# Performance work log

Measured on AMD Instinct MI355X. Metric: run time of the kernel, lower is better.

## Reference

```python
import jax, jax.numpy as jnp
import numpy as np

M, D_H, D_K, D_V = 8, 512, 64, 64
B, N = 16, 1024

def _xavier(key, shape, gain=1.414):
    fan_in, fan_out = shape[-2], shape[-1]
    limit = gain * (6.0 / (fan_in + fan_out)) ** 0.5
    return jax.random.uniform(key, shape, jnp.float32, -limit, limit)

def setup_inputs() -> dict:
    key = jax.random.key(0)
    kH, kq, kk, kv, ko = jax.random.split(key, 5)
    return {
        "H": jax.random.normal(kH, (B, N, D_H), jnp.float32),
        "W_Q": _xavier(kq, (M, D_H, D_K)),
        "W_K": _xavier(kk, (M, D_H, D_K)),
        "W_V": _xavier(kv, (M, D_H, D_V)),
        "W_O": _xavier(ko, (M, D_V, D_H)),
    }

def reference(H, W_Q, W_K, W_V, W_O):
    # H: [B, n, d_h]; per-head projections -> [B, M, n, d_k/d_v]
    Q = jnp.einsum('bnd,mdq->bmnq', H, W_Q)
    K = jnp.einsum('bnd,mdk->bmnk', H, W_K)
    V = jnp.einsum('bnd,mdv->bmnv', H, W_V)
    scale = 1.0 / jnp.sqrt(jnp.float32(W_K.shape[-1]))
    U = scale * jnp.einsum('bmnq,bmkq->bmnk', Q, K)  # [B, M, n, n]
    A = jax.nn.softmax(U, axis=-1)
    Hp = jnp.einsum('bmnk,bmkv->bmnv', A, V)          # [B, M, n, d_v]
    # per-head output projection then sum over heads (dim=-3)
    return jnp.einsum('bmnv,mvd->bnd', Hp, W_O)       # [B, n, d_h]
```

## Files before the change

### kernel.cpp

```cpp
#include <hip/hip_runtime.h>
#include <hip/hip_bf16.h>

typedef __attribute__((ext_vector_type(8))) short bf16x8;
typedef __attribute__((ext_vector_type(4))) float f32x4;
typedef __attribute__((ext_vector_type(16))) float f32x16;
typedef __attribute__((ext_vector_type(2))) unsigned uint2v;

__device__ __forceinline__ ushort f2bf(float f) {
  union { float f; unsigned u; } v; v.f = f;
  unsigned r = v.u + 0x7FFFu + ((v.u >> 16) & 1u);
  return (ushort)(r >> 16);
}

__device__ __forceinline__ float exp2_(float x) {
#if __has_builtin(__builtin_amdgcn_exp2f)
  return __builtin_amdgcn_exp2f(x);
#else
  return exp2f(x);
#endif
}

__device__ __forceinline__ unsigned cvtpk(float lo, float hi) {
  unsigned r;
  asm("v_cvt_pk_bf16_f32 %0, %1, %2" : "=v"(r) : "v"(lo), "v"(hi));
  return r;
}

__device__ __forceinline__ uint2v lane32_swap(unsigned a, unsigned b) {
#if __has_builtin(__builtin_amdgcn_permlane32_swap)
  return __builtin_amdgcn_permlane32_swap(a, b, false, false);
#else
  unsigned sa = (unsigned)__shfl_xor((int)a, 32);
  unsigned sb = (unsigned)__shfl_xor((int)b, 32);
  bool lo = ((threadIdx.x & 32) == 0);
  uint2v r;
  r.x = lo ? a : sb;
  r.y = lo ? sa : b;
  return r;
#endif
}

#define QSCALE 0.18033688011112042f

__global__ void __launch_bounds__(256) cast_h_kernel(const float* __restrict__ src,
                                                     ushort* __restrict__ dst) {
  int i = (blockIdx.x * 256 + threadIdx.x) * 8;
  float4 a = *(const float4*)(src + i);
  float4 b = *(const float4*)(src + i + 4);
  uint4 o;
  o.x = f2bf(a.x) | ((unsigned)f2bf(a.y) << 16);
  o.y = f2bf(a.z) | ((unsigned)f2bf(a.w) << 16);
  o.z = f2bf(b.x) | ((unsigned)f2bf(b.y) << 16);
  o.w = f2bf(b.z) | ((unsigned)f2bf(b.w) << 16);
  *(uint4*)(dst + i) = o;
}

__global__ void __launch_bounds__(256) pack_wqkv_kernel(const float* __restrict__ WQ,
                                                        const float* __restrict__ WK,
                                                        const float* __restrict__ WV,
                                                        ushort* __restrict__ dst) {
  int t = blockIdx.x * 256 + threadIdx.x;
  int j = t >> 9, d = t & 511;
  int m = j / 192, r = j % 192, which = r >> 6, dk = r & 63;
  const float* W = (which == 0) ? WQ : (which == 1) ? WK : WV;
  dst[t] = f2bf(W[(m * 512 + d) * 64 + dk]);
}

__global__ void __launch_bounds__(256) pack_wo_kernel(const float* __restrict__ WO,
                                                      ushort* __restrict__ dst) {
  int t = blockIdx.x * 256 + threadIdx.x;
  int j = t >> 9, mv = t & 511;
  dst[t] = f2bf(WO[mv * 512 + j]);
}

template <int EPI>
__global__ void __launch_bounds__(256) gemm_bt_kernel(
    const ushort* __restrict__ A, const ushort* __restrict__ Bt,
    float* __restrict__ C, int Kdim, int Ncols,
    ushort* __restrict__ Qo, ushort* __restrict__ Ko, ushort* __restrict__ Vo) {
  __shared__ __align__(16) ushort As[128][72];
  __shared__ __align__(16) ushort Bs[128][72];
  const int tid = threadIdx.x;
  const int lane = tid & 63, w = tid >> 6;
  const int wr = w >> 1, wc = w & 1;
  const int brow = blockIdx.y * 128, bcol = blockIdx.x * 128;

  f32x4 acc[4][4];
  const f32x4 z4 = {0.f, 0.f, 0.f, 0.f};
#pragma unroll
  for (int i = 0; i < 4; ++i)
#pragma unroll
    for (int j = 0; j < 4; ++j) acc[i][j] = z4;

  for (int k0 = 0; k0 < Kdim; k0 += 64) {
    __syncthreads();
#pragma unroll
    for (int i = 0; i < 4; ++i) {
      int c = tid + i * 256;
      int row = c >> 3, cc = (c & 7) * 8;
      *(uint4*)&As[row][cc] = *(const uint4*)(A + (size_t)(brow + row) * Kdim + k0 + cc);
      *(uint4*)&Bs[row][cc] = *(const uint4*)(Bt + (size_t)(bcol + row) * Kdim + k0 + cc);
    }
    __syncthreads();
#pragma unroll
    for (int kk = 0; kk < 64; kk += 32) {
      bf16x8 a[4], b[4];
#pragma unroll
      for (int i = 0; i < 4; ++i)
        a[i] = *(const bf16x8*)&As[wr * 64 + i * 16 + (lane & 15)][kk + (lane >> 4) * 8];
#pragma unroll
      for (int j = 0; j < 4; ++j)
        b[j] = *(const bf16x8*)&Bs[wc * 64 + j * 16 + (lane & 15)][kk + (lane >> 4) * 8];
#pragma unroll
      for (int i = 0; i < 4; ++i)
#pragma unroll
        for (int j = 0; j < 4; ++j)
          acc[i][j] = __builtin_amdgcn_mfma_f32_16x16x32_bf16(a[i], b[j], acc[i][j], 0, 0, 0);
    }
  }

#pragma unroll
  for (int i = 0; i < 4; ++i) {
    int row0 = brow + wr * 64 + i * 16 + (lane >> 4) * 4;
#pragma unroll
    for (int j = 0; j < 4; ++j) {
      int col = bcol + wc * 64 + j * 16 + (lane & 15);
      if (EPI == 0) {
#pragma unroll
        for (int q = 0; q < 4; ++q)
          C[(size_t)(row0 + q) * Ncols + col] = acc[i][j][q];
      } else {
        int m = col / 192, r = col % 192, which = r >> 6, dk = r & 63;
        ushort* base = (which == 0) ? Qo : (which == 1) ? Ko : Vo;
        float cs = (which == 0) ? QSCALE : 1.0f;
#pragma unroll
        for (int q = 0; q < 4; ++q) {
          int row = row0 + q;
          int b = row >> 10, n = row & 1023;
          base[(size_t)((b * 8 + m) * 1024 + n) * 64 + dk] = f2bf(acc[i][j][q] * cs);
        }
      }
    }
  }
}

__global__ void __launch_bounds__(256) transpose_v_kernel(const ushort* __restrict__ V,
                                                          ushort* __restrict__ Vt) {
  __shared__ __align__(16) ushort T[64][72];
  int bm = blockIdx.x >> 4, nt = blockIdx.x & 15;
  const ushort* src = V + (size_t)bm * 65536 + nt * 64 * 64;
  int tid = threadIdx.x;
#pragma unroll
  for (int i = 0; i < 2; ++i) {
    int c = tid + i * 256;
    int row = c >> 3, cc = (c & 7) * 8;
    *(uint4*)&T[row][cc] = *(const uint4*)(src + c * 8);
  }
  __syncthreads();
  int v = tid >> 2, nn0 = (tid & 3) * 16;
  ushort tmp[16];
#pragma unroll
  for (int k = 0; k < 16; ++k) tmp[k] = T[nn0 + k][v];
  ushort* dst = Vt + (size_t)bm * 65536 + v * 1024 + nt * 64 + nn0;
  *(uint4*)(dst + 0) = *(uint4*)&tmp[0];
  *(uint4*)(dst + 8) = *(uint4*)&tmp[8];
}

__global__ void __launch_bounds__(256, 2) attn_kernel(const ushort* __restrict__ Q,
                                                      const ushort* __restrict__ K,
                                                      const ushort* __restrict__ Vt,
                                                      ushort* __restrict__ Hp) {
  __shared__ __align__(16) ushort Ks[2][64 * 64];
  __shared__ __align__(16) ushort Vs[2][64 * 64];

  int wk = (blockIdx.x & 7) * 64 + (blockIdx.x >> 3);
  const int bm = wk >> 2, qt = wk & 3;
  const int b = bm >> 3, m = bm & 7;
  const int tid = threadIdx.x, lane = tid & 63, w = tid >> 6;
  const int hi = lane >> 5, l31 = lane & 31;
  const ushort* Qp = Q + (size_t)bm * 65536;
  const ushort* Kp = K + (size_t)bm * 65536;
  const ushort* Vp = Vt + (size_t)bm * 65536;
  const int qw = qt * 256 + w * 64;

  bf16x8 qb[2][4];
#pragma unroll
  for (int qs = 0; qs < 2; ++qs)
#pragma unroll
    for (int s = 0; s < 4; ++s)
      qb[qs][s] = *(const bf16x8*)(Qp + (size_t)(qw + qs * 32 + l31) * 64 + s * 16 + hi * 8);

  f32x16 oacc[2][2];
#pragma unroll
  for (int qs = 0; qs < 2; ++qs)
#pragma unroll
    for (int vj = 0; vj < 2; ++vj)
#pragma unroll
      for (int r = 0; r < 16; ++r) oacc[qs][vj][r] = 0.f;
  float mrun[2] = {-1e30f, -1e30f}, lrun[2] = {0.f, 0.f};

  const int sr = tid >> 2, sc4 = (tid & 3) << 4;
  const unsigned bo0 = ((unsigned)(sc4 * 2)) ^ (((unsigned)(sr & 7)) << 4);

  {
    uint4 k0 = *(const uint4*)(Kp + (size_t)sr * 64 + sc4);
    uint4 k1 = *(const uint4*)(Kp + (size_t)sr * 64 + sc4 + 8);
    uint4 v0 = *(const uint4*)(Vp + (size_t)sr * 1024 + sc4);
    uint4 v1 = *(const uint4*)(Vp + (size_t)sr * 1024 + sc4 + 8);
    char* kd = (char*)&Ks[0][sr * 64];
    char* vd = (char*)&Vs[0][sr * 64];
    *(uint4*)(kd + bo0) = k0; *(uint4*)(kd + (bo0 ^ 16)) = k1;
    *(uint4*)(vd + bo0) = v0; *(uint4*)(vd + (bo0 ^ 16)) = v1;
  }
  __syncthreads();

  int cur = 0;
  for (int kt = 0; kt < 16; ++kt) {
    uint4 k0, k1, v0, v1;
    const bool pf = (kt < 15);
    if (pf) {
      int n0 = (kt + 1) * 64;
      k0 = *(const uint4*)(Kp + (size_t)(n0 + sr) * 64 + sc4);
      k1 = *(const uint4*)(Kp + (size_t)(n0 + sr) * 64 + sc4 + 8);
      v0 = *(const uint4*)(Vp + (size_t)sr * 1024 + n0 + sc4);
      v1 = *(const uint4*)(Vp + (size_t)sr * 1024 + n0 + sc4 + 8);
    }

    const ushort* kbase = &Ks[cur][0];
    bf16x8 kA[2][4];
#pragma unroll
    for (int ja = 0; ja < 2; ++ja) {
      int row = ja * 32 + l31;
      const char* kr = (const char*)(kbase + row * 64);
#pragma unroll
      for (int s = 0; s < 4; ++s)
        kA[ja][s] = *(const bf16x8*)(kr + (((unsigned)(s * 32 + hi * 16)) ^ (((unsigned)(row & 7)) << 4)));
    }

    f32x16 st[2][2];
#pragma unroll
    for (int qs = 0; qs < 2; ++qs)
#pragma unroll
      for (int ja = 0; ja < 2; ++ja) {
#pragma unroll
        for (int r = 0; r < 16; ++r) st[qs][ja][r] = 0.f;
#pragma unroll
        for (int s = 0; s < 4; ++s)
          st[qs][ja] = __builtin_amdgcn_mfma_f32_32x32x16_bf16(kA[ja][s], qb[qs][s], st[qs][ja], 0, 0, 0);
      }

    bf16x8 pb[2][4];
#pragma unroll
    for (int qs = 0; qs < 2; ++qs) {
      float tm[16];
#pragma unroll
      for (int r = 0; r < 16; ++r) tm[r] = fmaxf(st[qs][0][r], st[qs][1][r]);
#pragma unroll
      for (int sd = 8; sd >= 1; sd >>= 1)
#pragma unroll
        for (int r = 0; r < sd; ++r) tm[r] = fmaxf(tm[r], tm[r + sd]);
      float mx = fmaxf(tm[0], __shfl_xor(tm[0], 32));
      float mnew = fmaxf(mrun[qs], mx);
      float scal = exp2_(mrun[qs] - mnew);
      mrun[qs] = mnew;
#pragma unroll
      for (int ja = 0; ja < 2; ++ja)
#pragma unroll
        for (int r = 0; r < 16; ++r)
          st[qs][ja][r] = exp2_(st[qs][ja][r] - mnew);
      float ts[16];
#pragma unroll
      for (int r = 0; r < 16; ++r) ts[r] = st[qs][0][r] + st[qs][1][r];
#pragma unroll
      for (int sd = 8; sd >= 1; sd >>= 1)
#pragma unroll
        for (int r = 0; r < sd; ++r) ts[r] += ts[r + sd];
      float rs = ts[0] + __shfl_xor(ts[0], 32);
      lrun[qs] = lrun[qs] * scal + rs;
#pragma unroll
      for (int vj = 0; vj < 2; ++vj)
#pragma unroll
        for (int r = 0; r < 16; ++r) oacc[qs][vj][r] *= scal;

#pragma unroll
      for (int ja = 0; ja < 2; ++ja)
#pragma unroll
        for (int g = 0; g < 2; ++g) {
          unsigned x0 = cvtpk(st[qs][ja][g * 8 + 0], st[qs][ja][g * 8 + 1]);
          unsigned x1 = cvtpk(st[qs][ja][g * 8 + 2], st[qs][ja][g * 8 + 3]);
          unsigned y0 = cvtpk(st[qs][ja][g * 8 + 4], st[qs][ja][g * 8 + 5]);
          unsigned y1 = cvtpk(st[qs][ja][g * 8 + 6], st[qs][ja][g * 8 + 7]);
          uint2v s0 = lane32_swap(x0, y0);
          uint2v s1 = lane32_swap(x1, y1);
          uint4 wv; wv.x = s0.x; wv.y = s1.x; wv.z = s0.y; wv.w = s1.y;
          pb[qs][ja * 2 + g] = *(bf16x8*)&wv;
        }
    }

    const ushort* vbase = &Vs[cur][0];
#pragma unroll
    for (int vj = 0; vj < 2; ++vj) {
      int row = vj * 32 + l31;
      const char* vr = (const char*)(vbase + row * 64);
      bf16x8 va[4];
#pragma unroll
      for (int ks = 0; ks < 4; ++ks)
        va[ks] = *(const bf16x8*)(vr + (((unsigned)(ks * 32 + hi * 16)) ^ (((unsigned)(row & 7)) << 4)));
#pragma unroll
      for (int qs = 0; qs < 2; ++qs)
#pragma unroll
        for (int ks = 0; ks < 4; ++ks)
          oacc[qs][vj] = __builtin_amdgcn_mfma_f32_32x32x16_bf16(va[ks], pb[qs][ks], oacc[qs][vj], 0, 0, 0);
    }

    if (pf) {
      char* kd = (char*)&Ks[cur ^ 1][sr * 64];
      char* vd = (char*)&Vs[cur ^ 1][sr * 64];
      *(uint4*)(kd + bo0) = k0; *(uint4*)(kd + (bo0 ^ 16)) = k1;
      *(uint4*)(vd + bo0) = v0; *(uint4*)(vd + (bo0 ^ 16)) = v1;
    }
    __syncthreads();
    cur ^= 1;
  }

#pragma unroll
  for (int qs = 0; qs < 2; ++qs) {
    float linv = 1.0f / lrun[qs];
    int q = qw + qs * 32 + l31;
    size_t ro = ((size_t)b * 1024 + q) * 512 + m * 64;
#pragma unroll
    for (int vj = 0; vj < 2; ++vj)
#pragma unroll
      for (int t4 = 0; t4 < 4; ++t4) {
        ushort4 o;
        o.x = f2bf(oacc[qs][vj][t4 * 4 + 0] * linv);
        o.y = f2bf(oacc[qs][vj][t4 * 4 + 1] * linv);
        o.z = f2bf(oacc[qs][vj][t4 * 4 + 2] * linv);
        o.w = f2bf(oacc[qs][vj][t4 * 4 + 3] * linv);
        *(ushort4*)(Hp + ro + vj * 32 + t4 * 8 + hi * 4) = o;
      }
  }
}

extern "C" void kernel_launch(void* const* d_in, const int* in_sizes, int n_in,
                              void* d_out, int out_size, void* d_ws, size_t ws_size,
                              hipStream_t stream) {
  const float* H  = (const float*)d_in[0];
  const float* WQ = (const float*)d_in[1];
  const float* WK = (const float*)d_in[2];
  const float* WV = (const float*)d_in[3];
  const float* WO = (const float*)d_in[4];
  float* out = (float*)d_out;

  ushort* ws   = (ushort*)d_ws;
  ushort* Hb   = ws;
  ushort* Wqkv = Hb + 16384 * 512;
  ushort* Wo   = Wqkv + 1536 * 512;
  ushort* Qb   = Wo + 512 * 512;
  ushort* Kb   = Qb + 128 * 1024 * 64;
  ushort* Vb   = Kb + 128 * 1024 * 64;
  ushort* Vtb  = Vb + 128 * 1024 * 64;
  ushort* Hp   = Vtb + 128 * 1024 * 64;

  cast_h_kernel<<<4096, 256, 0, stream>>>(H, Hb);
  pack_wqkv_kernel<<<3072, 256, 0, stream>>>(WQ, WK, WV, Wqkv);
  pack_wo_kernel<<<1024, 256, 0, stream>>>(WO, Wo);
  gemm_bt_kernel<1><<<dim3(12, 128), 256, 0, stream>>>(Hb, Wqkv, nullptr, 512, 1536,
                                                       Qb, Kb, Vb);
  transpose_v_kernel<<<2048, 256, 0, stream>>>(Vb, Vtb);
  attn_kernel<<<512, 256, 0, stream>>>(Qb, Kb, Vtb, Hp);
  gemm_bt_kernel<0><<<dim3(4, 128), 256, 0, stream>>>(Hp, Wo, out, 512, 512,
                                                      nullptr, nullptr, nullptr);
}
```

Baseline: 137.6 us.

## Fuse V transpose into QKV GEMM, use LDS direct loads, lazy-rescale softmax

The QKV GEMM now writes V already transposed, which removes the separate transpose kernel and its round trip through memory. Its tile loads now go straight from global memory into LDS via global_load_lds, with an unpadded layout. The attention kernel halves the queries per wave and doubles the grid, raising occupancy to 3 blocks. It folds the running-max subtraction into the MFMA accumulator input and rescales only when the max exceeds a threshold of 10. The row sums are computed with an MFMA against a ones vector instead of shuffle reductions. The lazy rescaling relies on scores staying bounded, and the unpadded LDS layout in the GEMM may cause bank conflicts.

```diff
diff --git a/kernel.cpp b/kernel.cpp
--- a/kernel.cpp
+++ b/kernel.cpp
@@ -40,6 +40,12 @@
 #endif
 }
 
+__device__ __forceinline__ void gload_lds16(const ushort* g, ushort* l) {
+  __builtin_amdgcn_global_load_lds(
+      (const __attribute__((address_space(1))) void*)g,
+      (__attribute__((address_space(3))) void*)l, 16, 0, 0);
+}
+
 #define QSCALE 0.18033688011112042f
 
 __global__ void __launch_bounds__(256) cast_h_kernel(const float* __restrict__ src,
@@ -77,14 +83,19 @@
 __global__ void __launch_bounds__(256) gemm_bt_kernel(
     const ushort* __restrict__ A, const ushort* __restrict__ Bt,
     float* __restrict__ C, int Kdim, int Ncols,
-    ushort* __restrict__ Qo, ushort* __restrict__ Ko, ushort* __restrict__ Vo) {
-  __shared__ __align__(16) ushort As[128][72];
-  __shared__ __align__(16) ushort Bs[128][72];
+    ushort* __restrict__ Qo, ushort* __restrict__ Ko, ushort* __restrict__ Vto) {
+  __shared__ __align__(16) ushort As[128 * 64];
+  __shared__ __align__(16) ushort Bs[128 * 64];
   const int tid = threadIdx.x;
   const int lane = tid & 63, w = tid >> 6;
   const int wr = w >> 1, wc = w & 1;
   const int brow = blockIdx.y * 128, bcol = blockIdx.x * 128;
 
+  const int srow = w * 32 + (lane >> 3);
+  const int scol = (lane & 7) * 8;
+  const ushort* ga = A + (size_t)(brow + srow) * Kdim + scol;
+  const ushort* gb = Bt + (size_t)(bcol + srow) * Kdim + scol;
+
   f32x4 acc[4][4];
   const f32x4 z4 = {0.f, 0.f, 0.f, 0.f};
 #pragma unroll
@@ -95,11 +106,9 @@
   for (int k0 = 0; k0 < Kdim; k0 += 64) {
     __syncthreads();
 #pragma unroll
-    for (int i = 0; i < 4; ++i) {
-      int c = tid + i * 256;
-      int row = c >> 3, cc = (c & 7) * 8;
-      *(uint4*)&As[row][cc] = *(const uint4*)(A + (size_t)(brow + row) * Kdim + k0 + cc);
-      *(uint4*)&Bs[row][cc] = *(const uint4*)(Bt + (size_t)(bcol + row) * Kdim + k0 + cc);
+    for (int t = 0; t < 4; ++t) {
+      gload_lds16(ga + k0 + t * 8 * Kdim, &As[(w * 32 + t * 8) * 64]);
+      gload_lds16(gb + k0 + t * 8 * Kdim, &Bs[(w * 32 + t * 8) * 64]);
     }
     __syncthreads();
 #pragma unroll
@@ -107,10 +116,10 @@
       bf16x8 a[4], b[4];
 #pragma unroll
       for (int i = 0; i < 4; ++i)
-        a[i] = *(const bf16x8*)&As[wr * 64 + i * 16 + (lane & 15)][kk + (lane >> 4) * 8];
+        a[i] = *(const bf16x8*)&As[(wr * 64 + i * 16 + (lane & 15)) * 64 + kk + (lane >> 4) * 8];
 #pragma unroll
       for (int j = 0; j < 4; ++j)
-        b[j] = *(const bf16x8*)&Bs[wc * 64 + j * 16 + (lane & 15)][kk + (lane >> 4) * 8];
+        b[j] = *(const bf16x8*)&Bs[(wc * 64 + j * 16 + (lane & 15)) * 64 + kk + (lane >> 4) * 8];
 #pragma unroll
       for (int i = 0; i < 4; ++i)
 #pragma unroll
@@ -131,73 +140,56 @@
           C[(size_t)(row0 + q) * Ncols + col] = acc[i][j][q];
       } else {
         int m = col / 192, r = col % 192, which = r >> 6, dk = r & 63;
-        ushort* base = (which == 0) ? Qo : (which == 1) ? Ko : Vo;
-        float cs = (which == 0) ? QSCALE : 1.0f;
-#pragma unroll
-        for (int q = 0; q < 4; ++q) {
-          int row = row0 + q;
-          int b = row >> 10, n = row & 1023;
-          base[(size_t)((b * 8 + m) * 1024 + n) * 64 + dk] = f2bf(acc[i][j][q] * cs);
+        int bb = row0 >> 10, n = row0 & 1023;
+        if (which == 2) {
+          ushort4 o;
+          o.x = f2bf(acc[i][j][0]);
+          o.y = f2bf(acc[i][j][1]);
+          o.z = f2bf(acc[i][j][2]);
+          o.w = f2bf(acc[i][j][3]);
+          *(ushort4*)(Vto + ((size_t)(bb * 8 + m) << 16) + (size_t)dk * 1024 + n) = o;
+        } else {
+          ushort* base = (which == 0) ? Qo : Ko;
+          float cs = (which == 0) ? QSCALE : 1.0f;
+#pragma unroll
+          for (int q = 0; q < 4; ++q)
+            base[(size_t)((bb * 8 + m) * 1024 + (n + q)) * 64 + dk] = f2bf(acc[i][j][q] * cs);
         }
       }
     }
   }
 }
 
-__global__ void __launch_bounds__(256) transpose_v_kernel(const ushort* __restrict__ V,
-                                                          ushort* __restrict__ Vt) {
-  __shared__ __align__(16) ushort T[64][72];
-  int bm = blockIdx.x >> 4, nt = blockIdx.x & 15;
-  const ushort* src = V + (size_t)bm * 65536 + nt * 64 * 64;
-  int tid = threadIdx.x;
-#pragma unroll
-  for (int i = 0; i < 2; ++i) {
-    int c = tid + i * 256;
-    int row = c >> 3, cc = (c & 7) * 8;
-    *(uint4*)&T[row][cc] = *(const uint4*)(src + c * 8);
-  }
-  __syncthreads();
-  int v = tid >> 2, nn0 = (tid & 3) * 16;
-  ushort tmp[16];
-#pragma unroll
-  for (int k = 0; k < 16; ++k) tmp[k] = T[nn0 + k][v];
-  ushort* dst = Vt + (size_t)bm * 65536 + v * 1024 + nt * 64 + nn0;
-  *(uint4*)(dst + 0) = *(uint4*)&tmp[0];
-  *(uint4*)(dst + 8) = *(uint4*)&tmp[8];
-}
-
-__global__ void __launch_bounds__(256, 2) attn_kernel(const ushort* __restrict__ Q,
+__global__ void __launch_bounds__(256, 3) attn_kernel(const ushort* __restrict__ Q,
                                                       const ushort* __restrict__ K,
                                                       const ushort* __restrict__ Vt,
                                                       ushort* __restrict__ Hp) {
   __shared__ __align__(16) ushort Ks[2][64 * 64];
   __shared__ __align__(16) ushort Vs[2][64 * 64];
 
-  int wk = (blockIdx.x & 7) * 64 + (blockIdx.x >> 3);
-  const int bm = wk >> 2, qt = wk & 3;
+  int wk = (blockIdx.x & 7) * 128 + (blockIdx.x >> 3);
+  const int bm = wk >> 3, qt = wk & 7;
   const int b = bm >> 3, m = bm & 7;
   const int tid = threadIdx.x, lane = tid & 63, w = tid >> 6;
   const int hi = lane >> 5, l31 = lane & 31;
   const ushort* Qp = Q + (size_t)bm * 65536;
   const ushort* Kp = K + (size_t)bm * 65536;
   const ushort* Vp = Vt + (size_t)bm * 65536;
-  const int qw = qt * 256 + w * 64;
-
-  bf16x8 qb[2][4];
-#pragma unroll
-  for (int qs = 0; qs < 2; ++qs)
-#pragma unroll
-    for (int s = 0; s < 4; ++s)
-      qb[qs][s] = *(const bf16x8*)(Qp + (size_t)(qw + qs * 32 + l31) * 64 + s * 16 + hi * 8);
-
-  f32x16 oacc[2][2];
-#pragma unroll
-  for (int qs = 0; qs < 2; ++qs)
-#pragma unroll
-    for (int vj = 0; vj < 2; ++vj)
-#pragma unroll
-      for (int r = 0; r < 16; ++r) oacc[qs][vj][r] = 0.f;
-  float mrun[2] = {-1e30f, -1e30f}, lrun[2] = {0.f, 0.f};
+  const int qw = qt * 128 + w * 32;
+
+  bf16x8 qb[4];
+#pragma unroll
+  for (int s = 0; s < 4; ++s)
+    qb[s] = *(const bf16x8*)(Qp + (size_t)(qw + l31) * 64 + s * 16 + hi * 8);
+
+  bf16x8 ones;
+#pragma unroll
+  for (int j = 0; j < 8; ++j) ones[j] = (short)0x3F80;
+
+  f32x16 oacc[2], lacc;
+#pragma unroll
+  for (int r = 0; r < 16; ++r) { oacc[0][r] = 0.f; oacc[1][r] = 0.f; lacc[r] = 0.f; }
+  float mrun = 0.f;
 
   const int sr = tid >> 2, sc4 = (tid & 3) << 4;
   const unsigned bo0 = ((unsigned)(sc4 * 2)) ^ (((unsigned)(sr & 7)) << 4);
@@ -237,65 +229,60 @@
         kA[ja][s] = *(const bf16x8*)(kr + (((unsigned)(s * 32 + hi * 16)) ^ (((unsigned)(row & 7)) << 4)));
     }
 
-    f32x16 st[2][2];
-#pragma unroll
-    for (int qs = 0; qs < 2; ++qs)
-#pragma unroll
-      for (int ja = 0; ja < 2; ++ja) {
-#pragma unroll
-        for (int r = 0; r < 16; ++r) st[qs][ja][r] = 0.f;
-#pragma unroll
-        for (int s = 0; s < 4; ++s)
-          st[qs][ja] = __builtin_amdgcn_mfma_f32_32x32x16_bf16(kA[ja][s], qb[qs][s], st[qs][ja], 0, 0, 0);
+    f32x16 cin;
+#pragma unroll
+    for (int r = 0; r < 16; ++r) cin[r] = -mrun;
+    f32x16 st0 = __builtin_amdgcn_mfma_f32_32x32x16_bf16(kA[0][0], qb[0], cin, 0, 0, 0);
+    f32x16 st1 = __builtin_amdgcn_mfma_f32_32x32x16_bf16(kA[1][0], qb[0], cin, 0, 0, 0);
+#pragma unroll
+    for (int s = 1; s < 4; ++s) {
+      st0 = __builtin_amdgcn_mfma_f32_32x32x16_bf16(kA[0][s], qb[s], st0, 0, 0, 0);
+      st1 = __builtin_amdgcn_mfma_f32_32x32x16_bf16(kA[1][s], qb[s], st1, 0, 0, 0);
+    }
+
+    float t[8];
+#pragma unroll
+    for (int r = 0; r < 8; ++r)
+      t[r] = fmaxf(fmaxf(st0[r], st0[r + 8]), fmaxf(st1[r], st1[r + 8]));
+    t[0] = fmaxf(fmaxf(t[0], t[4]), fmaxf(t[1], t[5]));
+    t[2] = fmaxf(fmaxf(t[2], t[6]), fmaxf(t[3], t[7]));
+    float mx = fmaxf(t[0], t[2]);
+    mx = fmaxf(mx, __shfl_xor(mx, 32));
+
+    if (__any(mx > 10.f)) {
+      float d = (mx > 10.f) ? mx : 0.f;
+      float scal = exp2_(-d);
+      mrun += d;
+#pragma unroll
+      for (int r = 0; r < 16; ++r) { st0[r] -= d; st1[r] -= d; }
+#pragma unroll
+      for (int r = 0; r < 16; ++r) { oacc[0][r] *= scal; oacc[1][r] *= scal; }
+      lacc[0] *= scal;
+    }
+
+#pragma unroll
+    for (int r = 0; r < 16; ++r) { st0[r] = exp2_(st0[r]); st1[r] = exp2_(st1[r]); }
+
+    bf16x8 pb[4];
+#pragma unroll
+    for (int ja = 0; ja < 2; ++ja) {
+      const f32x16& sj = ja ? st1 : st0;
+#pragma unroll
+      for (int g = 0; g < 2; ++g) {
+        unsigned x0 = cvtpk(sj[g * 8 + 0], sj[g * 8 + 1]);
+        unsigned x1 = cvtpk(sj[g * 8 + 2], sj[g * 8 + 3]);
+        unsigned y0 = cvtpk(sj[g * 8 + 4], sj[g * 8 + 5]);
+        unsigned y1 = cvtpk(sj[g * 8 + 6], sj[g * 8 + 7]);
+        uint2v s0 = lane32_swap(x0, y0);
+        uint2v s1 = lane32_swap(x1, y1);
+        uint4 wv; wv.x = s0.x; wv.y = s1.x; wv.z = s0.y; wv.w = s1.y;
+        pb[ja * 2 + g] = *(bf16x8*)&wv;
       }
-
-    bf16x8 pb[2][4];
-#pragma unroll
-    for (int qs = 0; qs < 2; ++qs) {
-      float tm[16];
-#pragma unroll
-      for (int r = 0; r < 16; ++r) tm[r] = fmaxf(st[qs][0][r], st[qs][1][r]);
-#pragma unroll
-      for (int sd = 8; sd >= 1; sd >>= 1)
-#pragma unroll
-        for (int r = 0; r < sd; ++r) tm[r] = fmaxf(tm[r], tm[r + sd]);
-      float mx = fmaxf(tm[0], __shfl_xor(tm[0], 32));
-      float mnew = fmaxf(mrun[qs], mx);
-      float scal = exp2_(mrun[qs] - mnew);
-      mrun[qs] = mnew;
-#pragma unroll
-      for (int ja = 0; ja < 2; ++ja)
-#pragma unroll
-        for (int r = 0; r < 16; ++r)
-          st[qs][ja][r] = exp2_(st[qs][ja][r] - mnew);
-      float ts[16];
-#pragma unroll
-      for (int r = 0; r < 16; ++r) ts[r] = st[qs][0][r] + st[qs][1][r];
-#pragma unroll
-      for (int sd = 8; sd >= 1; sd >>= 1)
-#pragma unroll
-        for (int r = 0; r < sd; ++r) ts[r] += ts[r + sd];
-      float rs = ts[0] + __shfl_xor(ts[0], 32);
-      lrun[qs] = lrun[qs] * scal + rs;
-#pragma unroll
-      for (int vj = 0; vj < 2; ++vj)
-#pragma unroll
-        for (int r = 0; r < 16; ++r) oacc[qs][vj][r] *= scal;
-
-#pragma unroll
-      for (int ja = 0; ja < 2; ++ja)
-#pragma unroll
-        for (int g = 0; g < 2; ++g) {
-          unsigned x0 = cvtpk(st[qs][ja][g * 8 + 0], st[qs][ja][g * 8 + 1]);
-          unsigned x1 = cvtpk(st[qs][ja][g * 8 + 2], st[qs][ja][g * 8 + 3]);
-          unsigned y0 = cvtpk(st[qs][ja][g * 8 + 4], st[qs][ja][g * 8 + 5]);
-          unsigned y1 = cvtpk(st[qs][ja][g * 8 + 6], st[qs][ja][g * 8 + 7]);
-          uint2v s0 = lane32_swap(x0, y0);
-          uint2v s1 = lane32_swap(x1, y1);
-          uint4 wv; wv.x = s0.x; wv.y = s1.x; wv.z = s0.y; wv.w = s1.y;
-          pb[qs][ja * 2 + g] = *(bf16x8*)&wv;
-        }
-    }
+    }
+
+#pragma unroll
+    for (int ks = 0; ks < 4; ++ks)
+      lacc = __builtin_amdgcn_mfma_f32_32x32x16_bf16(ones, pb[ks], lacc, 0, 0, 0);
 
     const ushort* vbase = &Vs[cur][0];
 #pragma unroll
@@ -307,10 +294,8 @@
       for (int ks = 0; ks < 4; ++ks)
         va[ks] = *(const bf16x8*)(vr + (((unsigned)(ks * 32 + hi * 16)) ^ (((unsigned)(row & 7)) << 4)));
 #pragma unroll
-      for (int qs = 0; qs < 2; ++qs)
-#pragma unroll
-        for (int ks = 0; ks < 4; ++ks)
-          oacc[qs][vj] = __builtin_amdgcn_mfma_f32_32x32x16_bf16(va[ks], pb[qs][ks], oacc[qs][vj], 0, 0, 0);
+      for (int ks = 0; ks < 4; ++ks)
+        oacc[vj] = __builtin_amdgcn_mfma_f32_32x32x16_bf16(va[ks], pb[ks], oacc[vj], 0, 0, 0);
     }
 
     if (pf) {
@@ -323,23 +308,20 @@
     cur ^= 1;
   }
 
-#pragma unroll
-  for (int qs = 0; qs < 2; ++qs) {
-    float linv = 1.0f / lrun[qs];
-    int q = qw + qs * 32 + l31;
-    size_t ro = ((size_t)b * 1024 + q) * 512 + m * 64;
-#pragma unroll
-    for (int vj = 0; vj < 2; ++vj)
-#pragma unroll
-      for (int t4 = 0; t4 < 4; ++t4) {
-        ushort4 o;
-        o.x = f2bf(oacc[qs][vj][t4 * 4 + 0] * linv);
-        o.y = f2bf(oacc[qs][vj][t4 * 4 + 1] * linv);
-        o.z = f2bf(oacc[qs][vj][t4 * 4 + 2] * linv);
-        o.w = f2bf(oacc[qs][vj][t4 * 4 + 3] * linv);
-        *(ushort4*)(Hp + ro + vj * 32 + t4 * 8 + hi * 4) = o;
-      }
-  }
+  float linv = 1.0f / lacc[0];
+  int q = qw + l31;
+  size_t ro = ((size_t)b * 1024 + q) * 512 + m * 64;
+#pragma unroll
+  for (int vj = 0; vj < 2; ++vj)
+#pragma unroll
+    for (int t4 = 0; t4 < 4; ++t4) {
+      ushort4 o;
+      o.x = f2bf(oacc[vj][t4 * 4 + 0] * linv);
+      o.y = f2bf(oacc[vj][t4 * 4 + 1] * linv);
+      o.z = f2bf(oacc[vj][t4 * 4 + 2] * linv);
+      o.w = f2bf(oacc[vj][t4 * 4 + 3] * linv);
+      *(ushort4*)(Hp + ro + vj * 32 + t4 * 8 + hi * 4) = o;
+    }
 }
 
 extern "C" void kernel_launch(void* const* d_in, const int* in_sizes, int n_in,
@@ -358,17 +340,15 @@
   ushort* Wo   = Wqkv + 1536 * 512;
   ushort* Qb   = Wo + 512 * 512;
   ushort* Kb   = Qb + 128 * 1024 * 64;
-  ushort* Vb   = Kb + 128 * 1024 * 64;
-  ushort* Vtb  = Vb + 128 * 1024 * 64;
+  ushort* Vtb  = Kb + 128 * 1024 * 64;
   ushort* Hp   = Vtb + 128 * 1024 * 64;
 
   cast_h_kernel<<<4096, 256, 0, stream>>>(H, Hb);
   pack_wqkv_kernel<<<3072, 256, 0, stream>>>(WQ, WK, WV, Wqkv);
   pack_wo_kernel<<<1024, 256, 0, stream>>>(WO, Wo);
   gemm_bt_kernel<1><<<dim3(12, 128), 256, 0, stream>>>(Hb, Wqkv, nullptr, 512, 1536,
-                                                       Qb, Kb, Vb);
-  transpose_v_kernel<<<2048, 256, 0, stream>>>(Vb, Vtb);
-  attn_kernel<<<512, 256, 0, stream>>>(Qb, Kb, Vtb, Hp);
+                                                       Qb, Kb, Vtb);
+  attn_kernel<<<1024, 256, 0, stream>>>(Qb, Kb, Vtb, Hp);
   gemm_bt_kernel<0><<<dim3(4, 128), 256, 0, stream>>>(Hp, Wo, out, 512, 512,
                                                       nullptr, nullptr, nullptr);
 }
```

Measured after the change: 141.7 us. +3.0%, slower.

## Fuse prep kernels, use direct global-to-LDS loads in GEMM, lazy softmax rescale

Applied to the files above, without the earlier changes.

Merges the three cast/pack kernels into one launch to cut launch overhead. The GEMM tile loads now go straight from global memory into LDS via global_load_lds and drop the padded LDS layout. The attention kernel folds the running max into the MFMA accumulator init and rescales only when the max grows past a threshold, which removes the per-tile exp and rescale of the accumulators. The unpadded LDS layout may add bank conflicts, and the lazy max relies on scores staying within a bounded range.

```diff
diff --git a/kernel.cpp b/kernel.cpp
--- a/kernel.cpp
+++ b/kernel.cpp
@@ -40,37 +40,41 @@
 #endif
 }
 
+__device__ __forceinline__ void gload_lds16(const ushort* g, ushort* l) {
+  __builtin_amdgcn_global_load_lds(
+      (const __attribute__((address_space(1))) void*)g,
+      (__attribute__((address_space(3))) void*)l, 16, 0, 0);
+}
+
 #define QSCALE 0.18033688011112042f
 
-__global__ void __launch_bounds__(256) cast_h_kernel(const float* __restrict__ src,
-                                                     ushort* __restrict__ dst) {
-  int i = (blockIdx.x * 256 + threadIdx.x) * 8;
-  float4 a = *(const float4*)(src + i);
-  float4 b = *(const float4*)(src + i + 4);
-  uint4 o;
-  o.x = f2bf(a.x) | ((unsigned)f2bf(a.y) << 16);
-  o.y = f2bf(a.z) | ((unsigned)f2bf(a.w) << 16);
-  o.z = f2bf(b.x) | ((unsigned)f2bf(b.y) << 16);
-  o.w = f2bf(b.z) | ((unsigned)f2bf(b.w) << 16);
-  *(uint4*)(dst + i) = o;
-}
-
-__global__ void __launch_bounds__(256) pack_wqkv_kernel(const float* __restrict__ WQ,
-                                                        const float* __restrict__ WK,
-                                                        const float* __restrict__ WV,
-                                                        ushort* __restrict__ dst) {
-  int t = blockIdx.x * 256 + threadIdx.x;
-  int j = t >> 9, d = t & 511;
-  int m = j / 192, r = j % 192, which = r >> 6, dk = r & 63;
-  const float* W = (which == 0) ? WQ : (which == 1) ? WK : WV;
-  dst[t] = f2bf(W[(m * 512 + d) * 64 + dk]);
-}
-
-__global__ void __launch_bounds__(256) pack_wo_kernel(const float* __restrict__ WO,
-                                                      ushort* __restrict__ dst) {
-  int t = blockIdx.x * 256 + threadIdx.x;
-  int j = t >> 9, mv = t & 511;
-  dst[t] = f2bf(WO[mv * 512 + j]);
+__global__ void __launch_bounds__(256) prep_kernel(
+    const float* __restrict__ H, const float* __restrict__ WQ,
+    const float* __restrict__ WK, const float* __restrict__ WV,
+    const float* __restrict__ WO, ushort* __restrict__ Hb,
+    ushort* __restrict__ Wqkv, ushort* __restrict__ Wo) {
+  int bid = blockIdx.x;
+  if (bid < 4096) {
+    int i = (bid * 256 + threadIdx.x) * 8;
+    float4 a = *(const float4*)(H + i);
+    float4 b = *(const float4*)(H + i + 4);
+    uint4 o;
+    o.x = f2bf(a.x) | ((unsigned)f2bf(a.y) << 16);
+    o.y = f2bf(a.z) | ((unsigned)f2bf(a.w) << 16);
+    o.z = f2bf(b.x) | ((unsigned)f2bf(b.y) << 16);
+    o.w = f2bf(b.z) | ((unsigned)f2bf(b.w) << 16);
+    *(uint4*)(Hb + i) = o;
+  } else if (bid < 7168) {
+    int t = (bid - 4096) * 256 + threadIdx.x;
+    int j = t >> 9, d = t & 511;
+    int m = j / 192, r = j % 192, which = r >> 6, dk = r & 63;
+    const float* W = (which == 0) ? WQ : (which == 1) ? WK : WV;
+    Wqkv[t] = f2bf(W[(m * 512 + d) * 64 + dk]);
+  } else {
+    int t = (bid - 7168) * 256 + threadIdx.x;
+    int j = t >> 9, mv = t & 511;
+    Wo[t] = f2bf(WO[mv * 512 + j]);
+  }
 }
 
 template <int EPI>
@@ -78,13 +82,18 @@
     const ushort* __restrict__ A, const ushort* __restrict__ Bt,
     float* __restrict__ C, int Kdim, int Ncols,
     ushort* __restrict__ Qo, ushort* __restrict__ Ko, ushort* __restrict__ Vo) {
-  __shared__ __align__(16) ushort As[128][72];
-  __shared__ __align__(16) ushort Bs[128][72];
+  __shared__ __align__(16) ushort As[128 * 64];
+  __shared__ __align__(16) ushort Bs[128 * 64];
   const int tid = threadIdx.x;
   const int lane = tid & 63, w = tid >> 6;
   const int wr = w >> 1, wc = w & 1;
   const int brow = blockIdx.y * 128, bcol = blockIdx.x * 128;
 
+  const int srow = w * 32 + (lane >> 3);
+  const int scol = (lane & 7) * 8;
+  const ushort* ga = A + (size_t)(brow + srow) * Kdim + scol;
+  const ushort* gb = Bt + (size_t)(bcol + srow) * Kdim + scol;
+
   f32x4 acc[4][4];
   const f32x4 z4 = {0.f, 0.f, 0.f, 0.f};
 #pragma unroll
@@ -95,11 +104,9 @@
   for (int k0 = 0; k0 < Kdim; k0 += 64) {
     __syncthreads();
 #pragma unroll
-    for (int i = 0; i < 4; ++i) {
-      int c = tid + i * 256;
-      int row = c >> 3, cc = (c & 7) * 8;
-      *(uint4*)&As[row][cc] = *(const uint4*)(A + (size_t)(brow + row) * Kdim + k0 + cc);
-      *(uint4*)&Bs[row][cc] = *(const uint4*)(Bt + (size_t)(bcol + row) * Kdim + k0 + cc);
+    for (int t = 0; t < 4; ++t) {
+      gload_lds16(ga + k0 + t * 8 * Kdim, &As[(w * 32 + t * 8) * 64]);
+      gload_lds16(gb + k0 + t * 8 * Kdim, &Bs[(w * 32 + t * 8) * 64]);
     }
     __syncthreads();
 #pragma unroll
@@ -107,10 +114,10 @@
       bf16x8 a[4], b[4];
 #pragma unroll
       for (int i = 0; i < 4; ++i)
-        a[i] = *(const bf16x8*)&As[wr * 64 + i * 16 + (lane & 15)][kk + (lane >> 4) * 8];
+        a[i] = *(const bf16x8*)&As[(wr * 64 + i * 16 + (lane & 15)) * 64 + kk + (lane >> 4) * 8];
 #pragma unroll
       for (int j = 0; j < 4; ++j)
-        b[j] = *(const bf16x8*)&Bs[wc * 64 + j * 16 + (lane & 15)][kk + (lane >> 4) * 8];
+        b[j] = *(const bf16x8*)&Bs[(wc * 64 + j * 16 + (lane & 15)) * 64 + kk + (lane >> 4) * 8];
 #pragma unroll
       for (int i = 0; i < 4; ++i)
 #pragma unroll
@@ -136,8 +143,8 @@
 #pragma unroll
         for (int q = 0; q < 4; ++q) {
           int row = row0 + q;
-          int b = row >> 10, n = row & 1023;
-          base[(size_t)((b * 8 + m) * 1024 + n) * 64 + dk] = f2bf(acc[i][j][q] * cs);
+          int bb = row >> 10, n = row & 1023;
+          base[(size_t)((bb * 8 + m) * 1024 + n) * 64 + dk] = f2bf(acc[i][j][q] * cs);
         }
       }
     }
@@ -192,12 +199,11 @@
 
   f32x16 oacc[2][2];
 #pragma unroll
-  for (int qs = 0; qs < 2; ++qs)
-#pragma unroll
-    for (int vj = 0; vj < 2; ++vj)
-#pragma unroll
-      for (int r = 0; r < 16; ++r) oacc[qs][vj][r] = 0.f;
-  float mrun[2] = {-1e30f, -1e30f}, lrun[2] = {0.f, 0.f};
+  for (int r = 0; r < 16; ++r) {
+    oacc[0][0][r] = 0.f; oacc[0][1][r] = 0.f;
+    oacc[1][0][r] = 0.f; oacc[1][1][r] = 0.f;
+  }
+  float mrun[2] = {0.f, 0.f}, lrun[2] = {0.f, 0.f};
 
   const int sr = tid >> 2, sc4 = (tid & 3) << 4;
   const unsigned bo0 = ((unsigned)(sc4 * 2)) ^ (((unsigned)(sr & 7)) << 4);
@@ -243,7 +249,7 @@
 #pragma unroll
       for (int ja = 0; ja < 2; ++ja) {
 #pragma unroll
-        for (int r = 0; r < 16; ++r) st[qs][ja][r] = 0.f;
+        for (int r = 0; r < 16; ++r) st[qs][ja][r] = -mrun[qs];
 #pragma unroll
         for (int s = 0; s < 4; ++s)
           st[qs][ja] = __builtin_amdgcn_mfma_f32_32x32x16_bf16(kA[ja][s], qb[qs][s], st[qs][ja], 0, 0, 0);
@@ -260,14 +266,24 @@
 #pragma unroll
         for (int r = 0; r < sd; ++r) tm[r] = fmaxf(tm[r], tm[r + sd]);
       float mx = fmaxf(tm[0], __shfl_xor(tm[0], 32));
-      float mnew = fmaxf(mrun[qs], mx);
-      float scal = exp2_(mrun[qs] - mnew);
-      mrun[qs] = mnew;
-#pragma unroll
-      for (int ja = 0; ja < 2; ++ja)
-#pragma unroll
-        for (int r = 0; r < 16; ++r)
-          st[qs][ja][r] = exp2_(st[qs][ja][r] - mnew);
+
+      if (__any(mx > 10.f)) {
+        float d = (mx > 10.f) ? mx : 0.f;
+        float scal = exp2_(-d);
+        mrun[qs] += d;
+#pragma unroll
+        for (int r = 0; r < 16; ++r) { st[qs][0][r] -= d; st[qs][1][r] -= d; }
+        lrun[qs] *= scal;
+#pragma unroll
+        for (int r = 0; r < 16; ++r) { oacc[qs][0][r] *= scal; oacc[qs][1][r] *= scal; }
+      }
+
+#pragma unroll
+      for (int r = 0; r < 16; ++r) {
+        st[qs][0][r] = exp2_(st[qs][0][r]);
+        st[qs][1][r] = exp2_(st[qs][1][r]);
+      }
+
       float ts[16];
 #pragma unroll
       for (int r = 0; r < 16; ++r) ts[r] = st[qs][0][r] + st[qs][1][r];
@@ -276,14 +292,10 @@
 #pragma unroll
         for (int r = 0; r < sd; ++r) ts[r] += ts[r + sd];
       float rs = ts[0] + __shfl_xor(ts[0], 32);
-      lrun[qs] = lrun[qs] * scal + rs;
-#pragma unroll
-      for (int vj = 0; vj < 2; ++vj)
-#pragma unroll
-        for (int r = 0; r < 16; ++r) oacc[qs][vj][r] *= scal;
-
-#pragma unroll
-      for (int ja = 0; ja < 2; ++ja)
+      lrun[qs] += rs;
+
+#pragma unroll
+      for (int ja = 0; ja < 2; ++ja) {
 #pragma unroll
         for (int g = 0; g < 2; ++g) {
           unsigned x0 = cvtpk(st[qs][ja][g * 8 + 0], st[qs][ja][g * 8 + 1]);
@@ -295,6 +307,7 @@
           uint4 wv; wv.x = s0.x; wv.y = s1.x; wv.z = s0.y; wv.w = s1.y;
           pb[qs][ja * 2 + g] = *(bf16x8*)&wv;
         }
+      }
     }
 
     const ushort* vbase = &Vs[cur][0];
@@ -362,9 +375,7 @@
   ushort* Vtb  = Vb + 128 * 1024 * 64;
   ushort* Hp   = Vtb + 128 * 1024 * 64;
 
-  cast_h_kernel<<<4096, 256, 0, stream>>>(H, Hb);
-  pack_wqkv_kernel<<<3072, 256, 0, stream>>>(WQ, WK, WV, Wqkv);
-  pack_wo_kernel<<<1024, 256, 0, stream>>>(WO, Wo);
+  prep_kernel<<<8192, 256, 0, stream>>>(H, WQ, WK, WV, WO, Hb, Wqkv, Wo);
   gemm_bt_kernel<1><<<dim3(12, 128), 256, 0, stream>>>(Hb, Wqkv, nullptr, 512, 1536,
                                                        Qb, Kb, Vb);
   transpose_v_kernel<<<2048, 256, 0, stream>>>(Vb, Vtb);
```

Result: no change. 136.5 us (-0.8%).
